# Kernel optimization log

Measured on AMD Instinct MI355X. Metric: run time of the kernel, lower is better.

## Reference

```python
import jax, jax.numpy as jnp
import numpy as np

LAYERS, BLOCKS = 10, 4
RES_CH, END_CH, CLASSES, GROUPS = 32, 256, 256, 1
BN_EPS = 1e-5


def conv1x1(x, w, b):
    # x: (bn, Cin, L), w: (Cout, Cin), b: (Cout,)
    return jnp.einsum('oc,bcl->bol', w, x) + b[None, :, None]


def mish(x):
    return x * jnp.tanh(jax.nn.softplus(x))


def concat_mish(x):
    return mish(jnp.concatenate((x, -x), axis=1))


def channel_shuffle(x, groups):
    if groups == 1:
        return x
    bn, c, l = x.shape
    return x.reshape(bn, groups, c // groups, l).transpose(0, 2, 1, 3).reshape(bn, c, l)


def batchnorm_train(x, g, b):
    # BatchNorm1d in training mode: per-channel stats over (batch, length), biased var
    m = jnp.mean(x, axis=(0, 2), keepdims=True)
    v = jnp.mean((x - m) ** 2, axis=(0, 2), keepdims=True)
    return (x - m) * jax.lax.rsqrt(v + BN_EPS) * g[None, :, None] + b[None, :, None]


def dilate(x, dilation, init_dilation, pad_start=True):
    bn, c, l = x.shape
    if dilation == 1:
        x = jnp.transpose(x, (1, 2, 0)).reshape(c, l * init_dilation, bn // init_dilation)
        return jnp.transpose(x, (2, 0, 1))
    f = dilation // init_dilation
    if f == 1:
        return x
    new_l = (l + f - 1) // f * f
    if new_l != l:
        pad = (new_l - l, 0) if pad_start else (0, new_l - l)
        x = jnp.pad(x, ((0, 0), (0, 0), pad))
        l = new_l
    l //= f
    bn *= f
    x = jnp.transpose(x, (1, 2, 0)).reshape(c, l, bn)
    return jnp.transpose(x, (2, 0, 1))


def setup_inputs() -> dict:
    key = jax.random.key(0)
    ks = iter(jax.random.split(key, 32))
    nl = LAYERS * BLOCKS
    f32 = jnp.float32
    inp = {
        'x': jax.random.normal(next(ks), (8, CLASSES, 8192), dtype=f32),
        'start_w': jax.random.normal(next(ks), (RES_CH, CLASSES), dtype=f32) * 0.05,
        'start_b': jnp.zeros((RES_CH,), f32),
        'gate_w': jax.random.normal(next(ks), (nl, RES_CH // 2, RES_CH), dtype=f32) * 0.15,
        'gate_b': jnp.zeros((nl, RES_CH // 2), f32),
        'res_w': jax.random.normal(next(ks), (nl, RES_CH, RES_CH), dtype=f32) * 0.15,
        'res_b': jnp.zeros((nl, RES_CH), f32),
        'bn_g': jnp.ones((nl, RES_CH), f32),
        'bn_b': jnp.zeros((nl, RES_CH), f32),
        'end_bn1_g': jnp.ones((RES_CH,), f32),
        'end_bn1_b': jnp.zeros((RES_CH,), f32),
        'end_conv1_w': jax.random.normal(next(ks), (END_CH // 2, 2 * RES_CH), dtype=f32) * 0.1,
        'end_conv1_b': jnp.zeros((END_CH // 2,), f32),
        'end_bn2_g': jnp.ones((END_CH // 2,), f32),
        'end_bn2_b': jnp.zeros((END_CH // 2,), f32),
        'end_conv2_w': jax.random.normal(next(ks), (CLASSES, END_CH), dtype=f32) * 0.05,
        'end_conv2_b': jnp.zeros((CLASSES,), f32),
    }
    return inp


def reference(x, start_w, start_b, gate_w, gate_b, res_w, res_b, bn_g, bn_b,
              end_bn1_g, end_bn1_b, end_conv1_w, end_conv1_b,
              end_bn2_g, end_bn2_b, end_conv2_w, end_conv2_b):
    x = conv1x1(x, start_w, start_b)
    prev_dilation = 1
    i = 0
    for block in range(BLOCKS):
        for layer in range(LAYERS):
            x = dilate(x, 2 ** layer, prev_dilation)
            prev_dilation = 2 ** layer
            x0 = x
            h = concat_mish(conv1x1(x, gate_w[i], gate_b[i]))
            h = channel_shuffle(h, GROUPS)
            h = batchnorm_train(conv1x1(h, res_w[i], res_b[i]), bn_g[i], bn_b[i])
            h = channel_shuffle(h, GROUPS)
            x = x0 + h
            i += 1
    x = concat_mish(batchnorm_train(x, end_bn1_g, end_bn1_b))
    x = concat_mish(batchnorm_train(conv1x1(x, end_conv1_w, end_conv1_b), end_bn2_g, end_bn2_b))
    x = conv1x1(x, end_conv2_w, end_conv2_b)
    x = dilate(x, 1, 2 ** (LAYERS - 1))
    return x
```

## Files before the change

kernel.cpp:

```cpp
#include <hip/hip_runtime.h>

#define BS 256
#define NBLKP 256
#define NBLK 256
#define NREP 64
#define SLOT_F 4096
#define STATS_F   0
#define W2T_F     184320
#define XBUF_F    262144
#define SYNC_F    2359296
#define WS_NEED_BYTES (4325376ull * 4ull)
#define CNTS_U  4096

__device__ __forceinline__ void mish2(float v, float& mp, float& mn) {
  float vc = fminf(fmaxf(v, -30.f), 30.f);
  float u  = __expf(vc);
  float n1 = u * (u + 2.f);
  mp = v * n1 * __builtin_amdgcn_rcpf(n1 + 2.f);
  float n2 = fmaf(2.f, u, 1.f);
  float d2 = fmaf(2.f * u, u, n2);
  mn = -v * n2 * __builtin_amdgcn_rcpf(d2);
}

__device__ __forceinline__ float coherent_ld(const float* p) {
  return __hip_atomic_load(p, __ATOMIC_RELAXED, __HIP_MEMORY_SCOPE_AGENT);
}
__device__ __forceinline__ void coherent_st(float* p, float v) {
  __hip_atomic_store(p, v, __ATOMIC_RELAXED, __HIP_MEMORY_SCOPE_AGENT);
}

__device__ __forceinline__ void block_reduce_stats(const float (&vals)[32],
    float* s_red, float* s_p2, float* slot, int t) {
  #pragma unroll
  for (int cc = 0; cc < 8; ++cc) {
    float4 v = make_float4(vals[cc*4+0], vals[cc*4+1], vals[cc*4+2], vals[cc*4+3]);
    *(float4*)(&s_red[t*32 + ((cc ^ (t & 7)) << 2)]) = v;
  }
  __syncthreads();
  {
    int q = t & 63, grp = t >> 6, c = q & 31;
    bool issq = (q >= 32);
    float acc = 0.f;
    #pragma clang loop unroll_count(8)
    for (int rr = 0; rr < 64; ++rr) {
      int row = grp * 64 + rr;
      float v = s_red[row*32 + ((((c >> 2) ^ (row & 7)) << 2) | (c & 3))];
      acc = fmaf(v, issq ? v : 1.f, acc);
    }
    s_p2[t] = acc;
  }
  __syncthreads();
  if (t < 64) {
    float tot = s_p2[t] + s_p2[t+64] + s_p2[t+128] + s_p2[t+192];
    unsafeAtomicAdd(&slot[(blockIdx.x & (NREP-1)) * 64 + t], tot);
  }
  __syncthreads();
}

__device__ __forceinline__ void bn32_from_slot(const float* slot, const float* g,
    const float* b, float* sA, float* sB, float* s_tmp, int t) {
  if (t < 64) {
    float s = 0.f;
    #pragma unroll
    for (int rep = 0; rep < NREP; ++rep) s += slot[rep*64 + t];
    s_tmp[t] = s;
  }
  __syncthreads();
  if (t < 32) {
    float mean = s_tmp[t] * (1.f/65536.f);
    float var  = fmaf(-mean, mean, s_tmp[t+32] * (1.f/65536.f));
    float sc   = g[t] * rsqrtf(var + 1e-5f);
    sA[t] = sc;
    sB[t] = fmaf(-mean, sc, b[t]);
  }
  __syncthreads();
}

__device__ __forceinline__ void bn32_slot_coh(const float* slot, const float* g,
    const float* b, float* sA, float* sB, float* s_tmp, int t) {
  if (t < 64) {
    float s = 0.f;
    #pragma unroll
    for (int rep = 0; rep < NREP; ++rep) s += coherent_ld(&slot[rep*64 + t]);
    s_tmp[t] = s;
  }
  __syncthreads();
  if (t < 32) {
    float mean = s_tmp[t] * (1.f/65536.f);
    float var  = fmaf(-mean, mean, s_tmp[t+32] * (1.f/65536.f));
    float sc   = g[t] * rsqrtf(var + 1e-5f);
    sA[t] = sc;
    sB[t] = fmaf(-mean, sc, b[t]);
  }
  __syncthreads();
}

__device__ __forceinline__ void layer_convs(const float (&x)[32], float (&r)[32],
    const float* gw, const float* gb, const float* rw, const float* rb, int i) {
  float g[16];
  #pragma unroll
  for (int j = 0; j < 16; ++j) g[j] = gb[i*16 + j];
  #pragma unroll
  for (int j = 0; j < 16; ++j)
    #pragma unroll
    for (int k = 0; k < 32; ++k)
      g[j] = fmaf(gw[i*512 + j*32 + k], x[k], g[j]);
  float cm[32];
  #pragma unroll
  for (int j = 0; j < 16; ++j) mish2(g[j], cm[j], cm[j+16]);
  #pragma unroll
  for (int j = 0; j < 32; ++j) r[j] = rb[i*32 + j];
  #pragma unroll
  for (int j = 0; j < 32; ++j)
    #pragma unroll
    for (int k = 0; k < 32; ++k)
      r[j] = fmaf(rw[i*1024 + j*32 + k], cm[k], r[j]);
}

__device__ __forceinline__ void grid_sync_lean(float* base, unsigned gen) {
  __syncthreads();
  unsigned* cnts = (unsigned*)base + CNTS_U;
  if (threadIdx.x == 0) {
    __hip_atomic_fetch_add(&cnts[(blockIdx.x & 31) * 16], 1u,
                           __ATOMIC_RELAXED, __HIP_MEMORY_SCOPE_AGENT);
    unsigned sum;
    do {
      __builtin_amdgcn_s_sleep(1);
      sum = 0;
      #pragma unroll
      for (int x = 0; x < 32; ++x)
        sum += __hip_atomic_load(&cnts[x*16], __ATOMIC_RELAXED, __HIP_MEMORY_SCOPE_AGENT);
    } while (sum < gen * NBLKP);
  }
  __syncthreads();
}

__device__ __forceinline__ void grid_sync_p(float* base, unsigned gen, bool flush) {
  __syncthreads();
  unsigned* flags = (unsigned*)base;
  unsigned* cnts  = (unsigned*)base + CNTS_U;
  if (blockIdx.x == 0) {
    if (threadIdx.x == 0) {
      if (flush) __threadfence();
      __hip_atomic_fetch_add(&cnts[0], 1u, __ATOMIC_RELAXED, __HIP_MEMORY_SCOPE_AGENT);
      unsigned sum;
      do {
        __builtin_amdgcn_s_sleep(2);
        sum = 0;
        #pragma unroll
        for (int x = 0; x < 32; ++x)
          sum += __hip_atomic_load(&cnts[x*16], __ATOMIC_RELAXED, __HIP_MEMORY_SCOPE_AGENT);
      } while (sum < gen * NBLK);
    }
    __syncthreads();
    __hip_atomic_store(&flags[threadIdx.x * 16], gen,
                       __ATOMIC_RELAXED, __HIP_MEMORY_SCOPE_AGENT);
  } else {
    if (threadIdx.x == 0) {
      if (flush) __threadfence();
      __hip_atomic_fetch_add(&cnts[(blockIdx.x & 31) * 16], 1u,
                             __ATOMIC_RELAXED, __HIP_MEMORY_SCOPE_AGENT);
      while (__hip_atomic_load(&flags[blockIdx.x * 16],
                               __ATOMIC_RELAXED, __HIP_MEMORY_SCOPE_AGENT) < gen)
        __builtin_amdgcn_s_sleep(2);
    }
    __syncthreads();
  }
}

extern "C" __global__ void __launch_bounds__(BS, 1)
qnet_p(const float* __restrict__ xin, const float* __restrict__ sw,
       const float* __restrict__ sb, const float* __restrict__ gw,
       const float* __restrict__ gb, const float* __restrict__ rw,
       const float* __restrict__ rb, const float* __restrict__ bng,
       const float* __restrict__ bnb, const float* __restrict__ e1g,
       const float* __restrict__ e1b, const float* __restrict__ c1w,
       const float* __restrict__ c1b, const float* __restrict__ c2w,
       float* __restrict__ ws)
{
  __shared__ float s_red[BS*32];
  __shared__ float s_p2[BS];
  __shared__ float s_A[32], s_B[32], s_tmp[64];
  const int t = threadIdx.x, p = blockIdx.x * BS + t;
  float* stats = ws + STATS_F;
  float* w2t   = ws + W2T_F;
  float* xb    = ws + XBUF_F;
  float* syncb = ws + SYNC_F;
  unsigned gen = 0;
  { int o = p & 255, kk = p >> 8; w2t[kk*256 + o] = c2w[o*256 + kk]; }
  const int bb = p >> 13, ll = p & 8191;
  const int pbase = bb * 2097152 + ll;
  float x[32];
  #pragma unroll
  for (int j = 0; j < 32; ++j) x[j] = sb[j];
  #pragma clang loop unroll(disable)
  for (int c8 = 0; c8 < 32; ++c8) {
    float xv[8];
    #pragma unroll
    for (int cc = 0; cc < 8; ++cc) xv[cc] = xin[pbase + (c8*8+cc)*8192];
    #pragma unroll
    for (int j = 0; j < 32; ++j)
      #pragma unroll
      for (int cc = 0; cc < 8; ++cc)
        x[j] = fmaf(sw[j*256 + c8*8 + cc], xv[cc], x[j]);
  }
  float r[32];
  layer_convs(x, r, gw, gb, rw, rb, 0);
  block_reduce_stats(r, s_red, s_p2, stats + 0, t);
  ++gen; grid_sync_lean(syncb, gen);
  #pragma clang loop unroll(disable)
  for (int i = 1; i < 40; ++i) {
    bn32_slot_coh(stats + (i-1)*SLOT_F, bng + (i-1)*32, bnb + (i-1)*32, s_A, s_B, s_tmp, t);
    #pragma unroll
    for (int c = 0; c < 32; ++c) x[c] += fmaf(r[c], s_A[c], s_B[c]);
    layer_convs(x, r, gw, gb, rw, rb, i);
    block_reduce_stats(r, s_red, s_p2, stats + i*SLOT_F, t);
    ++gen; grid_sync_lean(syncb, gen);
  }
  bn32_slot_coh(stats + 39*SLOT_F, bng + 39*32, bnb + 39*32, s_A, s_B, s_tmp, t);
  #pragma unroll
  for (int c = 0; c < 32; ++c) {
    x[c] += fmaf(r[c], s_A[c], s_B[c]);
    xb[c*65536 + p] = x[c];
  }
  block_reduce_stats(x, s_red, s_p2, stats + 40*SLOT_F, t);
  ++gen; grid_sync_lean(syncb, gen);
  bn32_slot_coh(stats + 40*SLOT_F, e1g, e1b, s_A, s_B, s_tmp, t);
  float mp[32], mn[32];
  #pragma unroll
  for (int c = 0; c < 32; ++c) {
    float xh = fmaf(x[c], s_A[c], s_B[c]);
    mish2(xh, mp[c], mn[c]);
  }
  #pragma clang loop unroll(disable)
  for (int pp = 0; pp < 4; ++pp) {
    float zc[32];
    #pragma unroll
    for (int j = 0; j < 32; ++j) zc[j] = c1b[pp*32 + j];
    #pragma unroll
    for (int j = 0; j < 32; ++j)
      #pragma unroll
      for (int k = 0; k < 32; ++k) {
        zc[j] = fmaf(c1w[(pp*32+j)*64 + k],      mp[k], zc[j]);
        zc[j] = fmaf(c1w[(pp*32+j)*64 + 32 + k], mn[k], zc[j]);
      }
    block_reduce_stats(zc, s_red, s_p2, stats + (41+pp)*SLOT_F, t);
  }
}

__global__ void __launch_bounds__(BS) k_end3(const float* __restrict__ e1g,
    const float* __restrict__ e1b, const float* __restrict__ c1w,
    const float* __restrict__ c1b, const float* __restrict__ e2g,
    const float* __restrict__ e2b, const float* __restrict__ c2b,
    float* __restrict__ out, float* __restrict__ ws) {
  __shared__ float s_A[32], s_B[32], s_tmp[64];
  __shared__ float s_A2[128], s_B2[128];
  __shared__ float s_ck[2048];
  __shared__ float s_c1b[128];
  __shared__ float s_c2b[64];
  int t = threadIdx.x, p = blockIdx.x * BS + t;
  float* stats = ws + STATS_F; float* xb = ws + XBUF_F;
  const float* w2t = ws + W2T_F;
  const int ocb = blockIdx.y * 64;
  if (t < 32) ((float4*)s_c1b)[t] = ((const float4*)c1b)[t];
  else if (t < 48) ((float4*)s_c2b)[t-32] = ((const float4*)(c2b + ocb))[t-32];
  bn32_from_slot(stats + 40*SLOT_F, e1g, e1b, s_A, s_B, s_tmp, t);
  if (t < 128) {
    int pp = t >> 5, c = t & 31;
    const float* sl = stats + (41+pp)*SLOT_F;
    float S = 0.f, Q = 0.f;
    #pragma unroll
    for (int rep = 0; rep < NREP; ++rep) { S += sl[rep*64 + c]; Q += sl[rep*64 + 32 + c]; }
    float mean = S * (1.f/65536.f);
    float var  = fmaf(-mean, mean, Q * (1.f/65536.f));
    float sc   = e2g[t] * rsqrtf(var + 1e-5f);
    s_A2[t] = sc;
    s_B2[t] = fmaf(-mean, sc, e2b[t]);
  }
  __syncthreads();
  float mp[32], mn[32];
  #pragma unroll
  for (int c = 0; c < 32; ++c) {
    float xh = fmaf(xb[c*65536 + p], s_A[c], s_B[c]);
    mish2(xh, mp[c], mn[c]);
  }
  float acc[64];
  #pragma unroll
  for (int o = 0; o < 64; ++o) acc[o] = s_c2b[o];
  #pragma clang loop unroll(disable)
  for (int kc = 0; kc < 4; ++kc) {
    __syncthreads();
    { const float4* cs = (const float4*)(c1w + kc*2048);
      ((float4*)s_ck)[t]       = cs[t];
      ((float4*)s_ck)[256 + t] = cs[256 + t]; }
    __syncthreads();
    #pragma clang loop unroll_count(2)
    for (int j = 0; j < 32; ++j) {
      const int k = kc*32 + j;
      float z = s_c1b[k];
      const float4* cw = (const float4*)&s_ck[j*64];
      #pragma unroll
      for (int k4 = 0; k4 < 8; ++k4) {
        float4 a = cw[k4], b = cw[8+k4];
        z = fmaf(a.x, mp[k4*4+0], z);
        z = fmaf(a.y, mp[k4*4+1], z);
        z = fmaf(a.z, mp[k4*4+2], z);
        z = fmaf(a.w, mp[k4*4+3], z);
        z = fmaf(b.x, mn[k4*4+0], z);
        z = fmaf(b.y, mn[k4*4+1], z);
        z = fmaf(b.z, mn[k4*4+2], z);
        z = fmaf(b.w, mn[k4*4+3], z);
      }
      float zh = fmaf(z, s_A2[k], s_B2[k]);
      float mpv, mnv; mish2(zh, mpv, mnv);
      const float* w0 = w2t + k*256 + ocb;
      const float* w1 = w2t + (k+128)*256 + ocb;
      #pragma unroll
      for (int o = 0; o < 64; ++o)
        acc[o] = fmaf(w0[o], mpv, fmaf(w1[o], mnv, acc[o]));
    }
  }
  int bb = p >> 13, ll = p & 8191;
  int obase = bb * 2097152 + ocb * 8192 + ll;
  #pragma unroll
  for (int o = 0; o < 64; ++o) out[obase + o*8192] = acc[o];
}

#define W2T_FB  4608
#define STATS_OUT_OFF (8u*1024u*1024u)
#define SLOT_STRIDE 16384

__device__ __forceinline__ void grid_sync_fb(float* ws, unsigned gen, bool flush) {
  grid_sync_p(ws, gen, flush);
}
__device__ __forceinline__ void brs_fb(const float (&vals)[32],
    float* s_red, float* s_p2, float* slot, int t) {
  #pragma unroll
  for (int cc = 0; cc < 8; ++cc) {
    float4 v = make_float4(vals[cc*4+0], vals[cc*4+1], vals[cc*4+2], vals[cc*4+3]);
    *(float4*)(&s_red[t*32 + ((cc ^ (t & 7)) << 2)]) = v;
  }
  __syncthreads();
  {
    int q = t & 63, grp = t >> 6, c = q & 31;
    bool issq = (q >= 32);
    float acc = 0.f;
    #pragma clang loop unroll_count(8)
    for (int rr = 0; rr < 64; ++rr) {
      int row = grp * 64 + rr;
      float v = s_red[row*32 + ((((c >> 2) ^ (row & 7)) << 2) | (c & 3))];
      acc = fmaf(v, issq ? v : 1.f, acc);
    }
    s_p2[t] = acc;
  }
  __syncthreads();
  if (t < 64) {
    float tot = s_p2[t] + s_p2[t+64] + s_p2[t+128] + s_p2[t+192];
    coherent_st(&slot[blockIdx.x * 64 + t], tot);
  }
}

extern "C" __global__ void __launch_bounds__(BS, 1)
qnet_fb(const float* __restrict__ xin,
        const float* __restrict__ sw, const float* __restrict__ sb,
        const float* __restrict__ gw, const float* __restrict__ gb,
        const float* __restrict__ rw, const float* __restrict__ rb,
        const float* __restrict__ bng, const float* __restrict__ bnb,
        const float* __restrict__ e1g, const float* __restrict__ e1b,
        const float* __restrict__ c1w, const float* __restrict__ c1b,
        const float* __restrict__ e2g, const float* __restrict__ e2b,
        const float* __restrict__ c2w, const float* __restrict__ c2b,
        float* __restrict__ out, float* __restrict__ ws)
{
  __shared__ float s_red[BS*32];
  __shared__ float s_p2[BS];
  __shared__ float s_tot[64];
  __shared__ float s_bcA[128];
  __shared__ float s_bcB[128];
  const int t = threadIdx.x;
  const int p = blockIdx.x * BS + t;
  float* w2t = ws + W2T_FB;
  float* zg  = out;
  float* sg  = out + STATS_OUT_OFF;
  unsigned gen = 0;
  const int bb = p >> 13, ll = p & 8191;
  const int pbase = bb * 2097152 + ll;
  { int o = p & 255, kk = p >> 8; coherent_st(&w2t[kk*256 + o], c2w[o*256 + kk]); }
  float x[32];
  #pragma unroll
  for (int j = 0; j < 32; ++j) x[j] = sb[j];
  #pragma clang loop unroll(disable)
  for (int c8 = 0; c8 < 32; ++c8) {
    float xv[8];
    #pragma unroll
    for (int cc = 0; cc < 8; ++cc) xv[cc] = xin[pbase + (c8*8+cc)*8192];
    #pragma unroll
    for (int j = 0; j < 32; ++j)
      #pragma unroll
      for (int cc = 0; cc < 8; ++cc)
        x[j] = fmaf(sw[j*256 + c8*8 + cc], xv[cc], x[j]);
  }
  #pragma clang loop unroll(disable)
  for (int i = 0; i < 40; ++i) {
    float r[32];
    layer_convs(x, r, gw, gb, rw, rb, i);
    brs_fb(r, s_red, s_p2, sg + (size_t)i * SLOT_STRIDE, t);
    ++gen; grid_sync_fb(ws, gen, false);
    {
      int q = t & 63, w = t >> 6;
      const float* col = sg + (size_t)i * SLOT_STRIDE + q;
      float acc2 = 0.f;
      #pragma clang loop unroll_count(16)
      for (int j = 0; j < 64; ++j) acc2 += coherent_ld(&col[(w*64+j)*64]);
      s_p2[t] = acc2;
    }
    __syncthreads();
    if (t < 64) s_tot[t] = s_p2[t] + s_p2[t+64] + s_p2[t+128] + s_p2[t+192];
    __syncthreads();
    if (t < 32) {
      float mean = s_tot[t] * (1.f/65536.f);
      float var  = fmaf(-mean, mean, s_tot[t+32] * (1.f/65536.f));
      float sc   = bng[i*32+t] * rsqrtf(var + 1e-5f);
      s_bcA[t] = sc;
      s_bcB[t] = fmaf(-mean, sc, bnb[i*32+t]);
    }
    __syncthreads();
    #pragma unroll
    for (int c = 0; c < 32; ++c) x[c] += fmaf(r[c], s_bcA[c], s_bcB[c]);
  }
  brs_fb(x, s_red, s_p2, sg + 40 * SLOT_STRIDE, t);
  ++gen; grid_sync_fb(ws, gen, false);
  {
    int q = t & 63, w = t >> 6;
    const float* col = sg + (size_t)40 * SLOT_STRIDE + q;
    float acc2 = 0.f;
    #pragma clang loop unroll_count(16)
    for (int j = 0; j < 64; ++j) acc2 += coherent_ld(&col[(w*64+j)*64]);
    s_p2[t] = acc2;
  }
  __syncthreads();
  if (t < 64) s_tot[t] = s_p2[t] + s_p2[t+64] + s_p2[t+128] + s_p2[t+192];
  __syncthreads();
  if (t < 32) {
    float mean = s_tot[t] * (1.f/65536.f);
    float var  = fmaf(-mean, mean, s_tot[t+32] * (1.f/65536.f));
    float sc   = e1g[t] * rsqrtf(var + 1e-5f);
    s_bcA[t] = sc;
    s_bcB[t] = fmaf(-mean, sc, e1b[t]);
  }
  __syncthreads();
  float mp[32], mn[32];
  #pragma unroll
  for (int c = 0; c < 32; ++c) {
    float xh = fmaf(x[c], s_bcA[c], s_bcB[c]);
    mish2(xh, mp[c], mn[c]);
  }
  #pragma clang loop unroll(disable)
  for (int pp = 0; pp < 4; ++pp) {
    float zc[32];
    #pragma unroll
    for (int j = 0; j < 32; ++j) zc[j] = c1b[pp*32 + j];
    #pragma unroll
    for (int j = 0; j < 32; ++j)
      #pragma unroll
      for (int k = 0; k < 32; ++k) {
        zc[j] = fmaf(c1w[(pp*32+j)*64 + k],      mp[k], zc[j]);
        zc[j] = fmaf(c1w[(pp*32+j)*64 + 32 + k], mn[k], zc[j]);
      }
    #pragma unroll
    for (int j = 0; j < 32; ++j) zg[(pp*32+j)*65536 + p] = zc[j];
    brs_fb(zc, s_red, s_p2, sg + (size_t)(41+pp) * SLOT_STRIDE, t);
    __syncthreads();
  }
  ++gen; grid_sync_fb(ws, gen, false);
  {
    int slot = 41 + (t >> 6), q = t & 63;
    const float* col = sg + (size_t)slot * SLOT_STRIDE + q;
    float acc2 = 0.f;
    #pragma clang loop unroll_count(32)
    for (int b2 = 0; b2 < 256; ++b2) acc2 += coherent_ld(&col[b2*64]);
    s_p2[t] = acc2;
  }
  __syncthreads();
  if (t < 128) {
    float S = s_p2[((t>>5)<<6) | (t&31)];
    float Q = s_p2[((t>>5)<<6) | 32 | (t&31)];
    float mean = S * (1.f/65536.f);
    float var  = fmaf(-mean, mean, Q * (1.f/65536.f));
    float sc   = e2g[t] * rsqrtf(var + 1e-5f);
    s_bcA[t] = sc;
    s_bcB[t] = fmaf(-mean, sc, e2b[t]);
  }
  __syncthreads();
  float acc[256];
  #pragma unroll
  for (int o = 0; o < 256; ++o) acc[o] = c2b[o];
  float zv_next = zg[p];
  #pragma clang loop unroll(disable)
  for (int k = 0; k < 128; ++k) {
    float zv = zv_next;
    zv_next = zg[((k+1)&127)*65536 + p];
    float zh = fmaf(zv, s_bcA[k], s_bcB[k]);
    float mpv, mnv; mish2(zh, mpv, mnv);
    const float* w0 = &w2t[k*256];
    const float* w1 = &w2t[(k+128)*256];
    #pragma unroll
    for (int o = 0; o < 256; ++o)
      acc[o] = fmaf(w0[o], mpv, fmaf(w1[o], mnv, acc[o]));
  }
  ++gen; grid_sync_fb(ws, gen, true);
  #pragma unroll
  for (int o = 0; o < 256; ++o)
    out[bb*2097152 + o*8192 + ll] = acc[o];
}

extern "C" void kernel_launch(void* const* d_in, const int* in_sizes, int n_in,
                              void* d_out, int out_size, void* d_ws, size_t ws_size,
                              hipStream_t stream) {
  const float* xin = (const float*)d_in[0];
  const float* sw  = (const float*)d_in[1];
  const float* sb  = (const float*)d_in[2];
  const float* gw  = (const float*)d_in[3];
  const float* gb  = (const float*)d_in[4];
  const float* rw  = (const float*)d_in[5];
  const float* rb  = (const float*)d_in[6];
  const float* bng = (const float*)d_in[7];
  const float* bnb = (const float*)d_in[8];
  const float* e1g = (const float*)d_in[9];
  const float* e1b = (const float*)d_in[10];
  const float* c1w = (const float*)d_in[11];
  const float* c1b = (const float*)d_in[12];
  const float* e2g = (const float*)d_in[13];
  const float* e2b = (const float*)d_in[14];
  const float* c2w = (const float*)d_in[15];
  const float* c2b = (const float*)d_in[16];
  float* out = (float*)d_out;
  float* ws  = (float*)d_ws;

  if (ws_size >= WS_NEED_BYTES) {
    hipMemsetAsync(d_ws, 0, 45 * SLOT_F * 4, stream);
    hipMemsetAsync((char*)d_ws + (size_t)SYNC_F * 4, 0, 4608 * 4, stream);
    void* args[] = { &xin, &sw, &sb, &gw, &gb, &rw, &rb, &bng, &bnb,
                     &e1g, &e1b, &c1w, &c1b, &c2w, &ws };
    hipError_t err = hipLaunchCooperativeKernel((const void*)qnet_p,
                                                dim3(NBLKP), dim3(BS), args, 0, stream);
    if (err != hipSuccess) {
      hipLaunchKernelGGL(qnet_p, dim3(NBLKP), dim3(BS), 0, stream,
                         xin, sw, sb, gw, gb, rw, rb, bng, bnb,
                         e1g, e1b, c1w, c1b, c2w, ws);
    }
    k_end3<<<dim3(256, 4), BS, 0, stream>>>(e1g, e1b, c1w, c1b, e2g, e2b, c2b, out, ws);
  } else {
    hipMemsetAsync(d_ws, 0, (CNTS_U + 512) * 4, stream);
    void* args[] = { &xin, &sw, &sb, &gw, &gb, &rw, &rb, &bng, &bnb,
                     &e1g, &e1b, &c1w, &c1b, &e2g, &e2b, &c2w, &c2b, &out, &ws };
    hipError_t err = hipLaunchCooperativeKernel((const void*)qnet_fb,
                                                dim3(NBLK), dim3(BS), args, 0, stream);
    if (err != hipSuccess) {
      hipLaunchKernelGGL(qnet_fb, dim3(NBLK), dim3(BS), 0, stream,
                         xin, sw, sb, gw, gb, rw, rb, bng, bnb,
                         e1g, e1b, c1w, c1b, e2g, e2b, c2w, c2b, out, ws);
    }
  }
}
```

Baseline: 1.550 ms.

## Stage conv2 weights in LDS and double persistent grid with idle helper blocks

In k_end3, each block now copies the 64-column slice of transposed conv2 weights for the current k-chunk into shared memory as float4. The inner accumulation then reads the weights with vector LDS loads instead of per-thread global loads. The persistent kernel is also launched with 512 blocks, where the extra 256 blocks duplicate the compute and take part in grid syncs but write no stats. The final BN read switches from the coherent loader to the plain slot loader. The larger grid may add grid-sync cost and duplicated work, and the extra 16KB of LDS may reduce occupancy in k_end3.

```diff
diff --git a/kernel.cpp b/kernel.cpp
--- a/kernel.cpp
+++ b/kernel.cpp
@@ -1,7 +1,7 @@
 #include <hip/hip_runtime.h>
 
 #define BS 256
-#define NBLKP 256
+#define NBLKP 512
 #define NBLK 256
 #define NREP 64
 #define SLOT_F 4096
@@ -187,8 +187,10 @@
   float* xb    = ws + XBUF_F;
   float* syncb = ws + SYNC_F;
   unsigned gen = 0;
-  { int o = p & 255, kk = p >> 8; w2t[kk*256 + o] = c2w[o*256 + kk]; }
-  const int bb = p >> 13, ll = p & 8191;
+  if (p < 65536) { int o = p & 255, kk = p >> 8; w2t[kk*256 + o] = c2w[o*256 + kk]; }
+  const bool worker = (blockIdx.x < 256);
+  const int wp = (p & 65535);
+  const int bb = wp >> 13, ll = wp & 8191;
   const int pbase = bb * 2097152 + ll;
   float x[32];
   #pragma unroll
@@ -206,7 +208,7 @@
   }
   float r[32];
   layer_convs(x, r, gw, gb, rw, rb, 0);
-  block_reduce_stats(r, s_red, s_p2, stats + 0, t);
+  if (worker) block_reduce_stats(r, s_red, s_p2, stats + 0, t);
   ++gen; grid_sync_lean(syncb, gen);
   #pragma clang loop unroll(disable)
   for (int i = 1; i < 40; ++i) {
@@ -214,18 +216,19 @@
     #pragma unroll
     for (int c = 0; c < 32; ++c) x[c] += fmaf(r[c], s_A[c], s_B[c]);
     layer_convs(x, r, gw, gb, rw, rb, i);
-    block_reduce_stats(r, s_red, s_p2, stats + i*SLOT_F, t);
+    if (worker) block_reduce_stats(r, s_red, s_p2, stats + i*SLOT_F, t);
     ++gen; grid_sync_lean(syncb, gen);
   }
   bn32_slot_coh(stats + 39*SLOT_F, bng + 39*32, bnb + 39*32, s_A, s_B, s_tmp, t);
   #pragma unroll
   for (int c = 0; c < 32; ++c) {
     x[c] += fmaf(r[c], s_A[c], s_B[c]);
-    xb[c*65536 + p] = x[c];
-  }
-  block_reduce_stats(x, s_red, s_p2, stats + 40*SLOT_F, t);
+    if (worker) xb[c*65536 + wp] = x[c];
+  }
+  if (worker) block_reduce_stats(x, s_red, s_p2, stats + 40*SLOT_F, t);
   ++gen; grid_sync_lean(syncb, gen);
-  bn32_slot_coh(stats + 40*SLOT_F, e1g, e1b, s_A, s_B, s_tmp, t);
+  if (!worker) return;
+  bn32_from_slot(stats + 40*SLOT_F, e1g, e1b, s_A, s_B, s_tmp, t);
   float mp[32], mn[32];
   #pragma unroll
   for (int c = 0; c < 32; ++c) {
@@ -256,6 +259,7 @@
   __shared__ float s_A[32], s_B[32], s_tmp[64];
   __shared__ float s_A2[128], s_B2[128];
   __shared__ float s_ck[2048];
+  __shared__ float4 wbuf4[1024];
   __shared__ float s_c1b[128];
   __shared__ float s_c2b[64];
   int t = threadIdx.x, p = blockIdx.x * BS + t;
@@ -293,6 +297,13 @@
     { const float4* cs = (const float4*)(c1w + kc*2048);
       ((float4*)s_ck)[t]       = cs[t];
       ((float4*)s_ck)[256 + t] = cs[256 + t]; }
+    #pragma unroll
+    for (int q = 0; q < 4; ++q) {
+      int f = q*256 + t;
+      int r = f >> 4, o4 = f & 15;
+      int kglob = (r < 32) ? (kc*32 + r) : (96 + kc*32 + r);
+      wbuf4[f] = *((const float4*)(w2t + kglob*256 + ocb) + o4);
+    }
     __syncthreads();
     #pragma clang loop unroll_count(2)
     for (int j = 0; j < 32; ++j) {
@@ -313,11 +324,16 @@
       }
       float zh = fmaf(z, s_A2[k], s_B2[k]);
       float mpv, mnv; mish2(zh, mpv, mnv);
-      const float* w0 = w2t + k*256 + ocb;
-      const float* w1 = w2t + (k+128)*256 + ocb;
-      #pragma unroll
-      for (int o = 0; o < 64; ++o)
-        acc[o] = fmaf(w0[o], mpv, fmaf(w1[o], mnv, acc[o]));
+      const float4* w0 = &wbuf4[j*16];
+      const float4* w1 = &wbuf4[(32 + j)*16];
+      #pragma unroll
+      for (int o4 = 0; o4 < 16; ++o4) {
+        float4 a = w0[o4], b = w1[o4];
+        acc[o4*4+0] = fmaf(a.x, mpv, fmaf(b.x, mnv, acc[o4*4+0]));
+        acc[o4*4+1] = fmaf(a.y, mpv, fmaf(b.y, mnv, acc[o4*4+1]));
+        acc[o4*4+2] = fmaf(a.z, mpv, fmaf(b.z, mnv, acc[o4*4+2]));
+        acc[o4*4+3] = fmaf(a.w, mpv, fmaf(b.w, mnv, acc[o4*4+3]));
+      }
     }
   }
   int bb = p >> 13, ll = p & 8191;
```

New measurement: 1.722 ms. 1.11x slower.
